# Performance work log

Hardware: AMD Instinct MI355X
Metric: run time of the kernel (lower is better)

The kernel has to match this reference:

```python
import jax, jax.numpy as jnp
import numpy as np

POOL = 7  # cfg.POOLING_SIZE


def roi_align_avg(feat, rois, scale):
    """Legacy RoIAlignAvg: bilinearly sample a (POOL+1)x(POOL+1) grid per RoI
    (crop_and_resize semantics: grid spans roi with divisor G-1), then 2x2
    average-pool with stride 1 -> POOL x POOL output. feat: [B,C,H,W]."""
    B, C, H, W = feat.shape
    G = POOL + 1
    b = rois[:, 0].astype(jnp.int32)                                  # [R]
    x1 = rois[:, 1] * scale
    y1 = rois[:, 2] * scale
    x2 = rois[:, 3] * scale
    y2 = rois[:, 4] * scale
    t = jnp.arange(G, dtype=feat.dtype) / (G - 1)                     # [G]
    ty = jnp.clip(y1[:, None] + (y2 - y1)[:, None] * t, 0.0, H - 1)   # [R,G] rows
    tx = jnp.clip(x1[:, None] + (x2 - x1)[:, None] * t, 0.0, W - 1)   # [R,G] cols
    y0f, x0f = jnp.floor(ty), jnp.floor(tx)
    wy = (ty - y0f)[:, :, None, None]                                 # row frac
    wx = (tx - x0f)[:, None, :, None]                                 # col frac
    y0 = y0f.astype(jnp.int32)
    x0 = x0f.astype(jnp.int32)
    y1i = jnp.minimum(y0 + 1, H - 1)
    x1i = jnp.minimum(x0 + 1, W - 1)

    def g(yi, xi):  # point gather -> [R,G,G,C]
        return feat[b[:, None, None], :, yi[:, :, None], xi[:, None, :]]

    v = ((1 - wy) * ((1 - wx) * g(y0, x0) + wx * g(y0, x1i))
         + wy * ((1 - wx) * g(y1i, x0) + wx * g(y1i, x1i)))           # [R,G,G,C]
    v = jnp.transpose(v, (0, 3, 1, 2))                                # [R,C,G,G]
    # 2x2 avg pool, stride 1 -> [R,C,POOL,POOL]
    return 0.25 * (v[:, :, :-1, :-1] + v[:, :, 1:, :-1]
                   + v[:, :, :-1, 1:] + v[:, :, 1:, 1:])


def reference(p2, p3, p4, p5, rois, im_info):
    """_PyramidRoI_Feat (POOLING_MODE='align'): data-dependent FPN level
    assignment per RoI, per-level RoIAlignAvg, reassembled in original RoI
    order (equivalent to the concat+sort in the torch code)."""
    h = rois[:, 4] - rois[:, 2] + 1.0
    w = rois[:, 3] - rois[:, 1] + 1.0
    lvl = jnp.floor(jnp.log(jnp.sqrt(h * w) / 224.0) / np.float32(np.log(2.0)) + 4.0)
    lvl = jnp.clip(lvl, 2.0, 5.0)                                     # [R]
    im_h = im_info[0, 0]
    out = 0.0
    for l, feat in zip((2, 3, 4, 5), (p2, p3, p4, p5)):
        scale = feat.shape[2] / im_h
        mask = (lvl == l).astype(feat.dtype)[:, None, None, None]
        out = out + mask * roi_align_avg(feat, rois, scale)
    return out  # [R, C, POOL, POOL]


def setup_inputs() -> dict:
    key = jax.random.key(0)
    ks = jax.random.split(key, 6)
    B, C = 1, 256
    IMH = IMW = 1024.0
    R = 2000
    p2 = jax.random.normal(ks[0], (B, C, 256, 256), jnp.float32)
    p3 = jax.random.normal(ks[1], (B, C, 128, 128), jnp.float32)
    p4 = jax.random.normal(ks[2], (B, C, 64, 64), jnp.float32)
    p5 = jax.random.normal(ks[3], (B, C, 32, 32), jnp.float32)
    # log-uniform box sizes so RoIs spread across all 4 pyramid levels
    wh = jnp.exp(jax.random.uniform(ks[4], (R, 2), jnp.float32,
                                    minval=np.log(16.0), maxval=np.log(600.0)))
    xy = jax.random.uniform(ks[5], (R, 2), jnp.float32) * (jnp.array([IMW, IMH]) - wh)
    rois = jnp.concatenate([
        jnp.zeros((R, 1), jnp.float32),            # batch index
        xy[:, 0:1], xy[:, 1:2],                    # x1, y1
        xy[:, 0:1] + wh[:, 0:1] - 1.0,             # x2
        xy[:, 1:2] + wh[:, 1:2] - 1.0,             # y2
    ], axis=1)
    im_info = jnp.array([[IMH, IMW, 1.0]], jnp.float32)
    return {"p2": p2, "p3": p3, "p4": p4, "p5": p5, "rois": rois, "im_info": im_info}
```

## Files before the change

kernel.cpp:

```cpp
#include <hip/hip_runtime.h>
#include <hip/hip_fp16.h>
#include <math.h>

#define POOLSZ 7
#define GRIDG 8
#define CCH  256
#define NBIN 256
#define OPP  (POOLSZ * POOLSZ)
#define MAXPER 8

typedef float fx4 __attribute__((ext_vector_type(4)));

__device__ __forceinline__ int roi_level(const float* __restrict__ rois, int r) {
    const float x1 = rois[r * 5 + 1];
    const float y1 = rois[r * 5 + 2];
    const float x2 = rois[r * 5 + 3];
    const float y2 = rois[r * 5 + 4];
    const float h = __fadd_rn(__fsub_rn(y2, y1), 1.0f);
    const float w = __fadd_rn(__fsub_rn(x2, x1), 1.0f);
    const float s = __fsqrt_rn(__fmul_rn(h, w));
    const float LOG2 = __uint_as_float(0x3F317218u);
    float lv = floorf(__fadd_rn(__fdiv_rn(logf(__fdiv_rn(s, 224.0f)), LOG2), 4.0f));
    lv = fminf(fmaxf(lv, 2.0f), 5.0f);
    return (int)lv;
}

__global__ __launch_bounds__(256) void prep_kernel(
    const float* __restrict__ p2, const float* __restrict__ p3,
    const float* __restrict__ p4, const float* __restrict__ p5,
    __half* __restrict__ t2, __half* __restrict__ t3,
    __half* __restrict__ t4, __half* __restrict__ t5,
    int HW2, int HW3, int HW4, int HW5,
    const float* __restrict__ rois, const float* __restrict__ im_info,
    int R, int* __restrict__ sorted, int nblkT)
{
    const int t = threadIdx.x;

    if ((int)blockIdx.x == nblkT) {
        __shared__ int cnt[NBIN];
        __shared__ int tmp[NBIN];
        cnt[t] = 0;
        __syncthreads();

        int myR[MAXPER], myBin[MAXPER], mySlot[MAXPER];
        int m = 0;
        const float ih = im_info[0], iw = im_info[1];
        for (int r = t; r < R && m < MAXPER; r += 256) {
            const int lvl = roi_level(rois, r);
            const float cx = 0.5f * (rois[r * 5 + 1] + rois[r * 5 + 3]);
            const float cy = 0.5f * (rois[r * 5 + 2] + rois[r * 5 + 4]);
            const int tx = min(7, max(0, (int)(cx * 8.0f / iw)));
            const int ty = min(7, max(0, (int)(cy * 8.0f / ih)));
            const int bin = (ty * 8 + tx) * 4 + (lvl - 2);
            myR[m] = r; myBin[m] = bin;
            mySlot[m] = atomicAdd(&cnt[bin], 1);
            ++m;
        }
        __syncthreads();

        const int v = cnt[t];
        tmp[t] = v;
        __syncthreads();
        for (int s = 1; s < NBIN; s <<= 1) {
            const int u = (t >= s) ? tmp[t - s] : 0;
            __syncthreads();
            tmp[t] += u;
            __syncthreads();
        }
        cnt[t] = tmp[t] - v;
        __syncthreads();

        for (int i = 0; i < m; ++i)
            sorted[cnt[myBin[i]] + mySlot[i]] = myR[i];
        return;
    }

    const int n2 = (HW2 / 64) * 4, n3 = (HW3 / 64) * 4, n4 = (HW4 / 64) * 4;
    int bid = blockIdx.x;
    const float* src; __half* dst; int HW;
    if (bid < n2)              { src = p2; dst = t2; HW = HW2; }
    else if ((bid -= n2) < n3) { src = p3; dst = t3; HW = HW3; }
    else if ((bid -= n3) < n4) { src = p4; dst = t4; HW = HW4; }
    else { bid -= n4;            src = p5; dst = t5; HW = HW5; }
    const int ptiles = HW / 64;
    const int pt = bid % ptiles, ct = bid / ptiles;
    const int pbase = pt * 64, cbase = ct * 64;

    __shared__ float tile[64][65];

    const int l = t & 15, cr = t >> 4;
#pragma unroll
    for (int p = 0; p < 4; ++p) {
        const int c = p * 16 + cr;
        const fx4* sp = (const fx4*)(src + (size_t)(cbase + c) * HW + pbase + l * 4);
        const fx4 v = __builtin_nontemporal_load(sp);
        tile[c][l * 4 + 0] = v.x;
        tile[c][l * 4 + 1] = v.y;
        tile[c][l * 4 + 2] = v.z;
        tile[c][l * 4 + 3] = v.w;
    }
    __syncthreads();

    const int ch2 = t & 31, pr = t >> 5;
#pragma unroll
    for (int p = 0; p < 8; ++p) {
        const int row = p * 8 + pr;
        const __half2 h = __floats2half2_rn(tile[ch2 * 2][row], tile[ch2 * 2 + 1][row]);
        *(__half2*)(dst + (size_t)(pbase + row) * CCH + cbase + ch2 * 2) = h;
    }
}

__global__ __launch_bounds__(256) void fpn_main_t(
    const __half* __restrict__ t2, const __half* __restrict__ t3,
    const __half* __restrict__ t4, const __half* __restrict__ t5,
    const float* __restrict__ rois, const float* __restrict__ im_info,
    float* __restrict__ out, const int* __restrict__ order,
    int H2, int H3, int H4, int H5, int R)
{
    const int n = blockIdx.x;
    const int q = R / 8, rem = R % 8;
    const int xcd = n % 8, idx = n / 8;
    const int nsw = (xcd < rem ? xcd * (q + 1) : rem * (q + 1) + (xcd - rem) * q) + idx;
    const int r = order ? order[nsw] : nsw;
    const int t = threadIdx.x;
    const int cpair = t & 127;
    const int grp   = t >> 7;
    const int c0    = cpair * 2;

    const float x1 = rois[r * 5 + 1];
    const float y1 = rois[r * 5 + 2];
    const float x2 = rois[r * 5 + 3];
    const float y2 = rois[r * 5 + 4];

    const int lvl = roi_level(rois, r);
    const __half* feat;
    int H;
    switch (lvl) {
        case 2:  feat = t2; H = H2; break;
        case 3:  feat = t3; H = H3; break;
        case 4:  feat = t4; H = H4; break;
        default: feat = t5; H = H5; break;
    }
    const int W = H;

    const float im_h  = im_info[0];
    const float scale = __fdiv_rn((float)H, im_h);
    const float ylo = __fmul_rn(y1, scale), yhi = __fmul_rn(y2, scale);
    const float xlo = __fmul_rn(x1, scale), xhi = __fmul_rn(x2, scale);

    float wx[GRIDG];
    int xoff[GRIDG], dxo[GRIDG];
#pragma unroll
    for (int i = 0; i < GRIDG; ++i) {
        const float tf = __fdiv_rn((float)i, (float)(GRIDG - 1));
        float tx = __fadd_rn(xlo, __fmul_rn(__fsub_rn(xhi, xlo), tf));
        tx = fminf(fmaxf(tx, 0.0f), (float)(W - 1));
        const float x0f = floorf(tx);
        const int   x0  = (int)x0f;
        xoff[i] = x0 * CCH;
        dxo[i]  = (min(x0 + 1, W - 1) - x0) * CCH;
        wx[i]   = __fsub_rn(tx, x0f);
    }

    float wyv[5];
    int yoff[5], dyo[5];
#pragma unroll
    for (int i = 0; i < 5; ++i) {
        const int gy = min(grp * 4 + i, GRIDG - 1);
        const float tf = __fdiv_rn((float)gy, (float)(GRIDG - 1));
        float ty = __fadd_rn(ylo, __fmul_rn(__fsub_rn(yhi, ylo), tf));
        ty = fminf(fmaxf(ty, 0.0f), (float)(H - 1));
        const float y0f = floorf(ty);
        const int   y0  = (int)y0f;
        yoff[i] = y0 * W * CCH;
        dyo[i]  = (min(y0 + 1, H - 1) - y0) * W * CCH;
        wyv[i]  = __fsub_rn(ty, y0f);
    }

    __shared__ float s_out[CCH * OPP];

    const __half* fb = feat + c0;
    float2 rowPrev[GRIDG], rowCur[GRIDG];
#pragma unroll
    for (int i = 0; i < 5; ++i) {
        if (grp == 1 && i == 4) break;
        const __half* base = fb + yoff[i];
        const int dyg = dyo[i];
        const float wyg = wyv[i];
        const float omy = 1.0f - wyg;
#pragma unroll
        for (int gx = 0; gx < GRIDG; ++gx) {
            const __half* qp = base + xoff[gx];
            const int dxg = dxo[gx];
            const float2 v00 = __half22float2(*(const __half2*)(qp));
            const float2 v01 = __half22float2(*(const __half2*)(qp + dxg));
            const float2 v10 = __half22float2(*(const __half2*)(qp + dyg));
            const float2 v11 = __half22float2(*(const __half2*)(qp + dyg + dxg));
            const float wxg = wx[gx];
            const float omx = 1.0f - wxg;
            rowCur[gx].x = omy * (omx * v00.x + wxg * v01.x)
                         + wyg * (omx * v10.x + wxg * v11.x);
            rowCur[gx].y = omy * (omx * v00.y + wxg * v01.y)
                         + wyg * (omx * v10.y + wxg * v11.y);
        }
        if (i > 0) {
            const int py = grp * 4 + i - 1;
#pragma unroll
            for (int px = 0; px < POOLSZ; ++px) {
                const float pvx = 0.25f * (rowPrev[px].x + rowPrev[px + 1].x
                                           + rowCur[px].x + rowCur[px + 1].x);
                const float pvy = 0.25f * (rowPrev[px].y + rowPrev[px + 1].y
                                           + rowCur[px].y + rowCur[px + 1].y);
                s_out[c0 * OPP + py * POOLSZ + px] = pvx;
                s_out[(c0 + 1) * OPP + py * POOLSZ + px] = pvy;
            }
        }
#pragma unroll
        for (int gx = 0; gx < GRIDG; ++gx) rowPrev[gx] = rowCur[gx];
    }

    __syncthreads();
    float* obase = out + (size_t)r * (CCH * OPP);
    const float* sp = s_out;
#pragma unroll
    for (int i = 0; i < 12; ++i) {
        const unsigned k4 = (unsigned)(i * 256 + t) * 4u;
        fx4 v;
        v.x = sp[k4 + 0]; v.y = sp[k4 + 1]; v.z = sp[k4 + 2]; v.w = sp[k4 + 3];
        __builtin_nontemporal_store(v, (fx4*)(obase + k4));
    }
    if (t < 64) {
        const unsigned k4 = (unsigned)(12 * 256 + t) * 4u;
        fx4 v;
        v.x = sp[k4 + 0]; v.y = sp[k4 + 1]; v.z = sp[k4 + 2]; v.w = sp[k4 + 3];
        __builtin_nontemporal_store(v, (fx4*)(obase + k4));
    }
}

__global__ __launch_bounds__(256) void fpn_roialign_kernel(
    const float* __restrict__ p2, const float* __restrict__ p3,
    const float* __restrict__ p4, const float* __restrict__ p5,
    const float* __restrict__ rois, const float* __restrict__ im_info,
    float* __restrict__ out,
    int H2, int H3, int H4, int H5, int R)
{
    const int r = blockIdx.x;

    const float bf = rois[r * 5 + 0];
    const float x1 = rois[r * 5 + 1];
    const float y1 = rois[r * 5 + 2];
    const float x2 = rois[r * 5 + 3];
    const float y2 = rois[r * 5 + 4];

    const int lvl = roi_level(rois, r);
    const float* feat;
    int H;
    switch (lvl) {
        case 2:  feat = p2; H = H2; break;
        case 3:  feat = p3; H = H3; break;
        case 4:  feat = p4; H = H4; break;
        default: feat = p5; H = H5; break;
    }
    const int W = H;
    const int wv  = threadIdx.x >> 6;
    const int lid = threadIdx.x & 63;
    const int gy  = lid >> 3;
    const int gx  = lid & 7;

    const float im_h  = im_info[0];
    const float scale = __fdiv_rn((float)H, im_h);
    const float ylo = __fmul_rn(y1, scale), yhi = __fmul_rn(y2, scale);
    const float xlo = __fmul_rn(x1, scale), xhi = __fmul_rn(x2, scale);
    float ty = __fadd_rn(ylo, __fmul_rn(__fsub_rn(yhi, ylo),
                                        __fdiv_rn((float)gy, (float)(GRIDG - 1))));
    ty = fminf(fmaxf(ty, 0.0f), (float)(H - 1));
    float tx = __fadd_rn(xlo, __fmul_rn(__fsub_rn(xhi, xlo),
                                        __fdiv_rn((float)gx, (float)(GRIDG - 1))));
    tx = fminf(fmaxf(tx, 0.0f), (float)(W - 1));
    const float y0f = floorf(ty), x0f = floorf(tx);
    const int   y0  = (int)y0f,   x0  = (int)x0f;
    const int   y1i = min(y0 + 1, H - 1);
    const int   x1i = min(x0 + 1, W - 1);
    const float wyv = __fsub_rn(ty, y0f);
    const float wxv = __fsub_rn(tx, x0f);
    const float omy = 1.0f - wyv;
    const float omx = 1.0f - wxv;

    const int b = (int)bf;
    const size_t plane = (size_t)H * W;
    const float* fbase = feat + (size_t)(b * CCH + wv * 64) * plane;
    const int o00 = y0  * W + x0;
    const int o01 = y0  * W + x1i;
    const int o10 = y1i * W + x0;
    const int o11 = y1i * W + x1i;

    float* obase = out + (size_t)r * (CCH * OPP) + (size_t)(wv * 64) * OPP;
    const bool wr  = (gy < POOLSZ) && (gx < POOLSZ);
    const int oidx = gy * POOLSZ + gx;

#pragma unroll 4
    for (int k = 0; k < 64; ++k) {
        const float* f = fbase + (size_t)k * plane;
        const float v00 = f[o00];
        const float v01 = f[o01];
        const float v10 = f[o10];
        const float v11 = f[o11];
        const float v = omy * (omx * v00 + wxv * v01) + wyv * (omx * v10 + wxv * v11);
        const float vb  = __shfl_down(v, 8);
        const float vr  = __shfl_down(v, 1);
        const float vbr = __shfl_down(v, 9);
        if (wr) obase[k * OPP + oidx] = 0.25f * (((v + vb) + vr) + vbr);
    }
}

extern "C" void kernel_launch(void* const* d_in, const int* in_sizes, int n_in,
                              void* d_out, int out_size, void* d_ws, size_t ws_size,
                              hipStream_t stream) {
    const float* p2      = (const float*)d_in[0];
    const float* p3      = (const float*)d_in[1];
    const float* p4      = (const float*)d_in[2];
    const float* p5      = (const float*)d_in[3];
    const float* rois    = (const float*)d_in[4];
    const float* im_info = (const float*)d_in[5];
    float* out = (float*)d_out;

    const int R = in_sizes[4] / 5;
    auto dimOf = [](int sz) {
        int hw = sz / CCH;
        return (int)(sqrtf((float)hw) + 0.5f);
    };
    const int H2 = dimOf(in_sizes[0]);
    const int H3 = dimOf(in_sizes[1]);
    const int H4 = dimOf(in_sizes[2]);
    const int H5 = dimOf(in_sizes[3]);
    const size_t HW2 = (size_t)H2 * H2, HW3 = (size_t)H3 * H3;
    const size_t HW4 = (size_t)H4 * H4, HW5 = (size_t)H5 * H5;

    const size_t sortBytes = (size_t)R * sizeof(int);
    const size_t sortPad   = (sortBytes + 255) & ~(size_t)255;
    const size_t transBytes = (HW2 + HW3 + HW4 + HW5) * CCH * sizeof(__half);
    const bool canSort  = (ws_size >= sortBytes) && (R <= 256 * MAXPER);
    const bool canTrans = ws_size >= sortPad + transBytes;

    if (canTrans) {
        int* sorted = canSort ? (int*)d_ws : nullptr;
        __half* t2 = (__half*)((char*)d_ws + sortPad);
        __half* t3 = t2 + HW2 * CCH;
        __half* t4 = t3 + HW3 * CCH;
        __half* t5 = t4 + HW4 * CCH;
        const int nblkT = (int)((HW2 + HW3 + HW4 + HW5) / 64 * 4);
        const int nblk  = nblkT + (canSort ? 1 : 0);
        prep_kernel<<<nblk, 256, 0, stream>>>(
            p2, p3, p4, p5, t2, t3, t4, t5,
            (int)HW2, (int)HW3, (int)HW4, (int)HW5,
            rois, im_info, R, sorted, nblkT);
        fpn_main_t<<<R, 256, 0, stream>>>(
            t2, t3, t4, t5, rois, im_info, out, sorted, H2, H3, H4, H5, R);
    } else {
        fpn_roialign_kernel<<<R, 256, 0, stream>>>(
            p2, p3, p4, p5, rois, im_info, out, H2, H3, H4, H5, R);
    }
}
```

Before: 62.07 us.

## Split prep into three kernels to overlap p2 transpose with coarse-level RoI work

The single prep kernel plus main kernel becomes three launches. The first sorts RoIs level-major and transposes p3-p5 to fp16 NHWC. The second interleaves p2 tile transposes with RoIAlign blocks for level 3-5 RoIs, and the third handles level-2 RoIs once p2 is ready. The aim is to hide the large p2 conversion behind useful RoI work rather than serializing all conversion before any sampling. The cost is an extra launch, idle early-exit blocks in k2 and k3, and a changed sort key that groups RoIs by level first.

```diff
diff --git a/kernel.cpp b/kernel.cpp
--- a/kernel.cpp
+++ b/kernel.cpp
@@ -25,104 +25,82 @@
     return (int)lv;
 }
 
-__global__ __launch_bounds__(256) void prep_kernel(
-    const float* __restrict__ p2, const float* __restrict__ p3,
-    const float* __restrict__ p4, const float* __restrict__ p5,
-    __half* __restrict__ t2, __half* __restrict__ t3,
-    __half* __restrict__ t4, __half* __restrict__ t5,
-    int HW2, int HW3, int HW4, int HW5,
-    const float* __restrict__ rois, const float* __restrict__ im_info,
-    int R, int* __restrict__ sorted, int nblkT)
-{
-    const int t = threadIdx.x;
-
-    if ((int)blockIdx.x == nblkT) {
-        __shared__ int cnt[NBIN];
-        __shared__ int tmp[NBIN];
-        cnt[t] = 0;
+__device__ __forceinline__ void do_sort(const float* __restrict__ rois,
+                                        const float* __restrict__ im_info,
+                                        int R, int* __restrict__ sorted,
+                                        int* __restrict__ meta, char* lds, int t)
+{
+    int* cnt = (int*)lds;
+    int* tmp = cnt + NBIN;
+    cnt[t] = 0;
+    __syncthreads();
+    int myR[MAXPER], myBin[MAXPER], mySlot[MAXPER];
+    int m = 0;
+    const float ih = im_info[0], iw = im_info[1];
+    for (int r = t; r < R && m < MAXPER; r += 256) {
+        const int lvl = roi_level(rois, r);
+        const float cx = 0.5f * (rois[r * 5 + 1] + rois[r * 5 + 3]);
+        const float cy = 0.5f * (rois[r * 5 + 2] + rois[r * 5 + 4]);
+        const int tx = min(7, max(0, (int)(cx * 8.0f / iw)));
+        const int ty = min(7, max(0, (int)(cy * 8.0f / ih)));
+        const int bin = (lvl - 2) * 64 + ty * 8 + tx;
+        myR[m] = r; myBin[m] = bin;
+        mySlot[m] = atomicAdd(&cnt[bin], 1);
+        ++m;
+    }
+    __syncthreads();
+    const int v = cnt[t];
+    tmp[t] = v;
+    __syncthreads();
+    for (int s = 1; s < NBIN; s <<= 1) {
+        const int u = (t >= s) ? tmp[t - s] : 0;
         __syncthreads();
-
-        int myR[MAXPER], myBin[MAXPER], mySlot[MAXPER];
-        int m = 0;
-        const float ih = im_info[0], iw = im_info[1];
-        for (int r = t; r < R && m < MAXPER; r += 256) {
-            const int lvl = roi_level(rois, r);
-            const float cx = 0.5f * (rois[r * 5 + 1] + rois[r * 5 + 3]);
-            const float cy = 0.5f * (rois[r * 5 + 2] + rois[r * 5 + 4]);
-            const int tx = min(7, max(0, (int)(cx * 8.0f / iw)));
-            const int ty = min(7, max(0, (int)(cy * 8.0f / ih)));
-            const int bin = (ty * 8 + tx) * 4 + (lvl - 2);
-            myR[m] = r; myBin[m] = bin;
-            mySlot[m] = atomicAdd(&cnt[bin], 1);
-            ++m;
-        }
+        tmp[t] += u;
         __syncthreads();
-
-        const int v = cnt[t];
-        tmp[t] = v;
-        __syncthreads();
-        for (int s = 1; s < NBIN; s <<= 1) {
-            const int u = (t >= s) ? tmp[t - s] : 0;
-            __syncthreads();
-            tmp[t] += u;
-            __syncthreads();
-        }
-        cnt[t] = tmp[t] - v;
-        __syncthreads();
-
-        for (int i = 0; i < m; ++i)
-            sorted[cnt[myBin[i]] + mySlot[i]] = myR[i];
-        return;
-    }
-
-    const int n2 = (HW2 / 64) * 4, n3 = (HW3 / 64) * 4, n4 = (HW4 / 64) * 4;
-    int bid = blockIdx.x;
-    const float* src; __half* dst; int HW;
-    if (bid < n2)              { src = p2; dst = t2; HW = HW2; }
-    else if ((bid -= n2) < n3) { src = p3; dst = t3; HW = HW3; }
-    else if ((bid -= n3) < n4) { src = p4; dst = t4; HW = HW4; }
-    else { bid -= n4;            src = p5; dst = t5; HW = HW5; }
+    }
+    cnt[t] = tmp[t] - v;
+    if (t == 64) meta[0] = cnt[64];
+    __syncthreads();
+    for (int i = 0; i < m; ++i)
+        sorted[cnt[myBin[i]] + mySlot[i]] = myR[i];
+}
+
+__device__ __forceinline__ void do_tile(const float* __restrict__ src,
+                                        __half* __restrict__ dst,
+                                        int HW, int jj, int t, char* lds)
+{
+    float* tile = (float*)lds;
     const int ptiles = HW / 64;
-    const int pt = bid % ptiles, ct = bid / ptiles;
+    const int pt = jj % ptiles, ct = jj / ptiles;
     const int pbase = pt * 64, cbase = ct * 64;
-
-    __shared__ float tile[64][65];
-
     const int l = t & 15, cr = t >> 4;
 #pragma unroll
     for (int p = 0; p < 4; ++p) {
         const int c = p * 16 + cr;
         const fx4* sp = (const fx4*)(src + (size_t)(cbase + c) * HW + pbase + l * 4);
         const fx4 v = __builtin_nontemporal_load(sp);
-        tile[c][l * 4 + 0] = v.x;
-        tile[c][l * 4 + 1] = v.y;
-        tile[c][l * 4 + 2] = v.z;
-        tile[c][l * 4 + 3] = v.w;
-    }
-    __syncthreads();
-
+        tile[c * 65 + l * 4 + 0] = v.x;
+        tile[c * 65 + l * 4 + 1] = v.y;
+        tile[c * 65 + l * 4 + 2] = v.z;
+        tile[c * 65 + l * 4 + 3] = v.w;
+    }
+    __syncthreads();
     const int ch2 = t & 31, pr = t >> 5;
 #pragma unroll
     for (int p = 0; p < 8; ++p) {
         const int row = p * 8 + pr;
-        const __half2 h = __floats2half2_rn(tile[ch2 * 2][row], tile[ch2 * 2 + 1][row]);
+        const __half2 h = __floats2half2_rn(tile[(ch2 * 2) * 65 + row],
+                                            tile[(ch2 * 2 + 1) * 65 + row]);
         *(__half2*)(dst + (size_t)(pbase + row) * CCH + cbase + ch2 * 2) = h;
     }
 }
 
-__global__ __launch_bounds__(256) void fpn_main_t(
-    const __half* __restrict__ t2, const __half* __restrict__ t3,
-    const __half* __restrict__ t4, const __half* __restrict__ t5,
+__device__ __forceinline__ void process_roi(
+    int r, const __half* __restrict__ feat, int H,
     const float* __restrict__ rois, const float* __restrict__ im_info,
-    float* __restrict__ out, const int* __restrict__ order,
-    int H2, int H3, int H4, int H5, int R)
-{
-    const int n = blockIdx.x;
-    const int q = R / 8, rem = R % 8;
-    const int xcd = n % 8, idx = n / 8;
-    const int nsw = (xcd < rem ? xcd * (q + 1) : rem * (q + 1) + (xcd - rem) * q) + idx;
-    const int r = order ? order[nsw] : nsw;
-    const int t = threadIdx.x;
+    float* __restrict__ out, char* lds, int t)
+{
+    const int W = H;
     const int cpair = t & 127;
     const int grp   = t >> 7;
     const int c0    = cpair * 2;
@@ -131,18 +109,6 @@
     const float y1 = rois[r * 5 + 2];
     const float x2 = rois[r * 5 + 3];
     const float y2 = rois[r * 5 + 4];
-
-    const int lvl = roi_level(rois, r);
-    const __half* feat;
-    int H;
-    switch (lvl) {
-        case 2:  feat = t2; H = H2; break;
-        case 3:  feat = t3; H = H3; break;
-        case 4:  feat = t4; H = H4; break;
-        default: feat = t5; H = H5; break;
-    }
-    const int W = H;
-
     const float im_h  = im_info[0];
     const float scale = __fdiv_rn((float)H, im_h);
     const float ylo = __fmul_rn(y1, scale), yhi = __fmul_rn(y2, scale);
@@ -177,7 +143,7 @@
         wyv[i]  = __fsub_rn(ty, y0f);
     }
 
-    __shared__ float s_out[CCH * OPP];
+    float* s_out = (float*)lds;
 
     const __half* fb = feat + c0;
     float2 rowPrev[GRIDG], rowCur[GRIDG];
@@ -237,6 +203,80 @@
     }
 }
 
+__global__ __launch_bounds__(256) void k1_kernel(
+    const float* __restrict__ p3, const float* __restrict__ p4,
+    const float* __restrict__ p5,
+    __half* __restrict__ t3, __half* __restrict__ t4, __half* __restrict__ t5,
+    int HW3, int HW4, int HW5,
+    const float* __restrict__ rois, const float* __restrict__ im_info,
+    int R, int* __restrict__ sorted, int* __restrict__ meta)
+{
+    __shared__ __align__(16) char lds[64 * 65 * 4];
+    const int t = threadIdx.x;
+    if (blockIdx.x == 0) {
+        do_sort(rois, im_info, R, sorted, meta, lds, t);
+        return;
+    }
+    int j = blockIdx.x - 1;
+    const int n5t = (HW5 / 64) * 4, n4t = (HW4 / 64) * 4;
+    if (j < n5t)                { do_tile(p5, t5, HW5, j, t, lds); return; }
+    if ((j -= n5t) < n4t)       { do_tile(p4, t4, HW4, j, t, lds); return; }
+    do_tile(p3, t3, HW3, j - n4t, t, lds);
+}
+
+__global__ __launch_bounds__(256) void k2_kernel(
+    const float* __restrict__ p2, __half* __restrict__ t2, int HW2,
+    const __half* __restrict__ t3, const __half* __restrict__ t4,
+    const __half* __restrict__ t5,
+    const float* __restrict__ rois, const float* __restrict__ im_info,
+    float* __restrict__ out, const int* __restrict__ sorted,
+    const int* __restrict__ meta,
+    int R, int H2, int H3, int H4, int H5)
+{
+    __shared__ __align__(16) char lds[CCH * OPP * 4];
+    const int t = threadIdx.x;
+    const long long NA = (HW2 / 64) * 4;
+    const long long N  = NA + R;
+    const long long i  = blockIdx.x;
+    const long long a0 = (i * NA) / N;
+    const long long a1 = ((i + 1) * NA) / N;
+    if (a1 > a0) {
+        do_tile(p2, t2, HW2, (int)a0, t, lds);
+        return;
+    }
+    const int k = (int)(i - a0);
+    const int n2 = meta[0];
+    const int n345 = R - n2;
+    if (k >= n345) return;
+    const int r = sorted[n2 + k];
+    const int lvl = roi_level(rois, r);
+    const __half* feat; int H;
+    switch (lvl) {
+        case 2:  feat = t2; H = H2; break;
+        case 3:  feat = t3; H = H3; break;
+        case 4:  feat = t4; H = H4; break;
+        default: feat = t5; H = H5; break;
+    }
+    process_roi(r, feat, H, rois, im_info, out, lds, t);
+}
+
+__global__ __launch_bounds__(256) void k3_kernel(
+    const __half* __restrict__ t2, int H2,
+    const float* __restrict__ rois, const float* __restrict__ im_info,
+    float* __restrict__ out, const int* __restrict__ sorted,
+    const int* __restrict__ meta, int R)
+{
+    __shared__ __align__(16) char lds[CCH * OPP * 4];
+    const int n2 = meta[0];
+    const int k = blockIdx.x;
+    if (k >= n2) return;
+    const int q = n2 / 8, rem = n2 % 8;
+    const int xcd = k % 8, idx = k / 8;
+    const int swz = (xcd < rem ? xcd * (q + 1) : rem * (q + 1) + (xcd - rem) * q) + idx;
+    const int r = sorted[swz];
+    process_roi(r, t2, H2, rois, im_info, out, lds, (int)threadIdx.x);
+}
+
 __global__ __launch_bounds__(256) void fpn_roialign_kernel(
     const float* __restrict__ p2, const float* __restrict__ p3,
     const float* __restrict__ p4, const float* __restrict__ p5,
@@ -245,7 +285,6 @@
     int H2, int H3, int H4, int H5, int R)
 {
     const int r = blockIdx.x;
-
     const float bf = rois[r * 5 + 0];
     const float x1 = rois[r * 5 + 1];
     const float y1 = rois[r * 5 + 2];
@@ -336,26 +375,31 @@
     const size_t HW2 = (size_t)H2 * H2, HW3 = (size_t)H3 * H3;
     const size_t HW4 = (size_t)H4 * H4, HW5 = (size_t)H5 * H5;
 
-    const size_t sortBytes = (size_t)R * sizeof(int);
-    const size_t sortPad   = (sortBytes + 255) & ~(size_t)255;
+    const size_t metaPad   = 256;
+    const size_t sortPad   = ((size_t)R * sizeof(int) + 255) & ~(size_t)255;
     const size_t transBytes = (HW2 + HW3 + HW4 + HW5) * CCH * sizeof(__half);
-    const bool canSort  = (ws_size >= sortBytes) && (R <= 256 * MAXPER);
-    const bool canTrans = ws_size >= sortPad + transBytes;
-
-    if (canTrans) {
-        int* sorted = canSort ? (int*)d_ws : nullptr;
-        __half* t2 = (__half*)((char*)d_ws + sortPad);
+    const bool canRun = (ws_size >= metaPad + sortPad + transBytes) && (R <= 256 * MAXPER);
+
+    if (canRun) {
+        int* meta   = (int*)d_ws;
+        int* sorted = (int*)((char*)d_ws + metaPad);
+        __half* t2 = (__half*)((char*)d_ws + metaPad + sortPad);
         __half* t3 = t2 + HW2 * CCH;
         __half* t4 = t3 + HW3 * CCH;
         __half* t5 = t4 + HW4 * CCH;
-        const int nblkT = (int)((HW2 + HW3 + HW4 + HW5) / 64 * 4);
-        const int nblk  = nblkT + (canSort ? 1 : 0);
-        prep_kernel<<<nblk, 256, 0, stream>>>(
-            p2, p3, p4, p5, t2, t3, t4, t5,
-            (int)HW2, (int)HW3, (int)HW4, (int)HW5,
-            rois, im_info, R, sorted, nblkT);
-        fpn_main_t<<<R, 256, 0, stream>>>(
-            t2, t3, t4, t5, rois, im_info, out, sorted, H2, H3, H4, H5, R);
+        const int n5t = (int)(HW5 / 64) * 4;
+        const int n4t = (int)(HW4 / 64) * 4;
+        const int n3t = (int)(HW3 / 64) * 4;
+        const int n2t = (int)(HW2 / 64) * 4;
+
+        k1_kernel<<<1 + n5t + n4t + n3t, 256, 0, stream>>>(
+            p3, p4, p5, t3, t4, t5, (int)HW3, (int)HW4, (int)HW5,
+            rois, im_info, R, sorted, meta);
+        k2_kernel<<<n2t + R, 256, 0, stream>>>(
+            p2, t2, (int)HW2, t3, t4, t5, rois, im_info, out, sorted, meta,
+            R, H2, H3, H4, H5);
+        k3_kernel<<<R, 256, 0, stream>>>(
+            t2, H2, rois, im_info, out, sorted, meta, R);
     } else {
         fpn_roialign_kernel<<<R, 256, 0, stream>>>(
             p2, p3, p4, p5, rois, im_info, out, H2, H3, H4, H5, R);
```

Result: slower. 77.65 us (+25.1%).

## Convert RoI main kernel to persistent blocks with atomic work queue

Applied to the files above, without the earlier changes.

Replaces the one-block-per-RoI launch with a persistent kernel of 768 blocks that pull sorted RoI indices from a global atomic counter, which is reset by a memset before the prep kernel. The goal is to balance the uneven per-level work dynamically and cut block launch overhead. It drops the XCD-aware swizzle of block indices, so locality across chiplets now depends on the dynamic order in which blocks claim work. It also adds an atomic plus two barriers per RoI and an extra memset call.

```diff
diff --git a/kernel.cpp b/kernel.cpp
--- a/kernel.cpp
+++ b/kernel.cpp
@@ -25,104 +25,81 @@
     return (int)lv;
 }
 
-__global__ __launch_bounds__(256) void prep_kernel(
-    const float* __restrict__ p2, const float* __restrict__ p3,
-    const float* __restrict__ p4, const float* __restrict__ p5,
-    __half* __restrict__ t2, __half* __restrict__ t3,
-    __half* __restrict__ t4, __half* __restrict__ t5,
-    int HW2, int HW3, int HW4, int HW5,
-    const float* __restrict__ rois, const float* __restrict__ im_info,
-    int R, int* __restrict__ sorted, int nblkT)
-{
-    const int t = threadIdx.x;
-
-    if ((int)blockIdx.x == nblkT) {
-        __shared__ int cnt[NBIN];
-        __shared__ int tmp[NBIN];
-        cnt[t] = 0;
+__device__ __forceinline__ void do_sort(const float* __restrict__ rois,
+                                        const float* __restrict__ im_info,
+                                        int R, int* __restrict__ sorted,
+                                        char* lds, int t)
+{
+    int* cnt = (int*)lds;
+    int* tmp = cnt + NBIN;
+    cnt[t] = 0;
+    __syncthreads();
+    int myR[MAXPER], myBin[MAXPER], mySlot[MAXPER];
+    int m = 0;
+    const float ih = im_info[0], iw = im_info[1];
+    for (int r = t; r < R && m < MAXPER; r += 256) {
+        const int lvl = roi_level(rois, r);
+        const float cx = 0.5f * (rois[r * 5 + 1] + rois[r * 5 + 3]);
+        const float cy = 0.5f * (rois[r * 5 + 2] + rois[r * 5 + 4]);
+        const int tx = min(7, max(0, (int)(cx * 8.0f / iw)));
+        const int ty = min(7, max(0, (int)(cy * 8.0f / ih)));
+        const int bin = (ty * 8 + tx) * 4 + (lvl - 2);
+        myR[m] = r; myBin[m] = bin;
+        mySlot[m] = atomicAdd(&cnt[bin], 1);
+        ++m;
+    }
+    __syncthreads();
+    const int v = cnt[t];
+    tmp[t] = v;
+    __syncthreads();
+    for (int s = 1; s < NBIN; s <<= 1) {
+        const int u = (t >= s) ? tmp[t - s] : 0;
         __syncthreads();
-
-        int myR[MAXPER], myBin[MAXPER], mySlot[MAXPER];
-        int m = 0;
-        const float ih = im_info[0], iw = im_info[1];
-        for (int r = t; r < R && m < MAXPER; r += 256) {
-            const int lvl = roi_level(rois, r);
-            const float cx = 0.5f * (rois[r * 5 + 1] + rois[r * 5 + 3]);
-            const float cy = 0.5f * (rois[r * 5 + 2] + rois[r * 5 + 4]);
-            const int tx = min(7, max(0, (int)(cx * 8.0f / iw)));
-            const int ty = min(7, max(0, (int)(cy * 8.0f / ih)));
-            const int bin = (ty * 8 + tx) * 4 + (lvl - 2);
-            myR[m] = r; myBin[m] = bin;
-            mySlot[m] = atomicAdd(&cnt[bin], 1);
-            ++m;
-        }
+        tmp[t] += u;
         __syncthreads();
-
-        const int v = cnt[t];
-        tmp[t] = v;
-        __syncthreads();
-        for (int s = 1; s < NBIN; s <<= 1) {
-            const int u = (t >= s) ? tmp[t - s] : 0;
-            __syncthreads();
-            tmp[t] += u;
-            __syncthreads();
-        }
-        cnt[t] = tmp[t] - v;
-        __syncthreads();
-
-        for (int i = 0; i < m; ++i)
-            sorted[cnt[myBin[i]] + mySlot[i]] = myR[i];
-        return;
-    }
-
-    const int n2 = (HW2 / 64) * 4, n3 = (HW3 / 64) * 4, n4 = (HW4 / 64) * 4;
-    int bid = blockIdx.x;
-    const float* src; __half* dst; int HW;
-    if (bid < n2)              { src = p2; dst = t2; HW = HW2; }
-    else if ((bid -= n2) < n3) { src = p3; dst = t3; HW = HW3; }
-    else if ((bid -= n3) < n4) { src = p4; dst = t4; HW = HW4; }
-    else { bid -= n4;            src = p5; dst = t5; HW = HW5; }
+    }
+    cnt[t] = tmp[t] - v;
+    __syncthreads();
+    for (int i = 0; i < m; ++i)
+        sorted[cnt[myBin[i]] + mySlot[i]] = myR[i];
+}
+
+__device__ __forceinline__ void do_tile(const float* __restrict__ src,
+                                        __half* __restrict__ dst,
+                                        int HW, int jj, int t, char* lds)
+{
+    float* tile = (float*)lds;
     const int ptiles = HW / 64;
-    const int pt = bid % ptiles, ct = bid / ptiles;
+    const int pt = jj % ptiles, ct = jj / ptiles;
     const int pbase = pt * 64, cbase = ct * 64;
-
-    __shared__ float tile[64][65];
-
     const int l = t & 15, cr = t >> 4;
 #pragma unroll
     for (int p = 0; p < 4; ++p) {
         const int c = p * 16 + cr;
         const fx4* sp = (const fx4*)(src + (size_t)(cbase + c) * HW + pbase + l * 4);
         const fx4 v = __builtin_nontemporal_load(sp);
-        tile[c][l * 4 + 0] = v.x;
-        tile[c][l * 4 + 1] = v.y;
-        tile[c][l * 4 + 2] = v.z;
-        tile[c][l * 4 + 3] = v.w;
-    }
-    __syncthreads();
-
+        tile[c * 65 + l * 4 + 0] = v.x;
+        tile[c * 65 + l * 4 + 1] = v.y;
+        tile[c * 65 + l * 4 + 2] = v.z;
+        tile[c * 65 + l * 4 + 3] = v.w;
+    }
+    __syncthreads();
     const int ch2 = t & 31, pr = t >> 5;
 #pragma unroll
     for (int p = 0; p < 8; ++p) {
         const int row = p * 8 + pr;
-        const __half2 h = __floats2half2_rn(tile[ch2 * 2][row], tile[ch2 * 2 + 1][row]);
+        const __half2 h = __floats2half2_rn(tile[(ch2 * 2) * 65 + row],
+                                            tile[(ch2 * 2 + 1) * 65 + row]);
         *(__half2*)(dst + (size_t)(pbase + row) * CCH + cbase + ch2 * 2) = h;
     }
 }
 
-__global__ __launch_bounds__(256) void fpn_main_t(
-    const __half* __restrict__ t2, const __half* __restrict__ t3,
-    const __half* __restrict__ t4, const __half* __restrict__ t5,
+__device__ __forceinline__ void process_roi(
+    int r, const __half* __restrict__ feat, int H,
     const float* __restrict__ rois, const float* __restrict__ im_info,
-    float* __restrict__ out, const int* __restrict__ order,
-    int H2, int H3, int H4, int H5, int R)
-{
-    const int n = blockIdx.x;
-    const int q = R / 8, rem = R % 8;
-    const int xcd = n % 8, idx = n / 8;
-    const int nsw = (xcd < rem ? xcd * (q + 1) : rem * (q + 1) + (xcd - rem) * q) + idx;
-    const int r = order ? order[nsw] : nsw;
-    const int t = threadIdx.x;
+    float* __restrict__ out, char* lds, int t)
+{
+    const int W = H;
     const int cpair = t & 127;
     const int grp   = t >> 7;
     const int c0    = cpair * 2;
@@ -131,18 +108,6 @@
     const float y1 = rois[r * 5 + 2];
     const float x2 = rois[r * 5 + 3];
     const float y2 = rois[r * 5 + 4];
-
-    const int lvl = roi_level(rois, r);
-    const __half* feat;
-    int H;
-    switch (lvl) {
-        case 2:  feat = t2; H = H2; break;
-        case 3:  feat = t3; H = H3; break;
-        case 4:  feat = t4; H = H4; break;
-        default: feat = t5; H = H5; break;
-    }
-    const int W = H;
-
     const float im_h  = im_info[0];
     const float scale = __fdiv_rn((float)H, im_h);
     const float ylo = __fmul_rn(y1, scale), yhi = __fmul_rn(y2, scale);
@@ -177,7 +142,7 @@
         wyv[i]  = __fsub_rn(ty, y0f);
     }
 
-    __shared__ float s_out[CCH * OPP];
+    float* s_out = (float*)lds;
 
     const __half* fb = feat + c0;
     float2 rowPrev[GRIDG], rowCur[GRIDG];
@@ -237,6 +202,61 @@
     }
 }
 
+__global__ __launch_bounds__(256) void prep_kernel(
+    const float* __restrict__ p2, const float* __restrict__ p3,
+    const float* __restrict__ p4, const float* __restrict__ p5,
+    __half* __restrict__ t2, __half* __restrict__ t3,
+    __half* __restrict__ t4, __half* __restrict__ t5,
+    int HW2, int HW3, int HW4, int HW5,
+    const float* __restrict__ rois, const float* __restrict__ im_info,
+    int R, int* __restrict__ sorted, int nblkT)
+{
+    __shared__ __align__(16) char lds[64 * 65 * 4];
+    const int t = threadIdx.x;
+    if ((int)blockIdx.x == nblkT) {
+        do_sort(rois, im_info, R, sorted, lds, t);
+        return;
+    }
+    const int n2 = (HW2 / 64) * 4, n3 = (HW3 / 64) * 4, n4 = (HW4 / 64) * 4;
+    int bid = blockIdx.x;
+    const float* src; __half* dst; int HW;
+    if (bid < n2)              { src = p2; dst = t2; HW = HW2; }
+    else if ((bid -= n2) < n3) { src = p3; dst = t3; HW = HW3; }
+    else if ((bid -= n3) < n4) { src = p4; dst = t4; HW = HW4; }
+    else { bid -= n4;            src = p5; dst = t5; HW = HW5; }
+    do_tile(src, dst, HW, bid, t, lds);
+}
+
+__global__ __launch_bounds__(256) void fpn_main_persist(
+    const __half* __restrict__ t2, const __half* __restrict__ t3,
+    const __half* __restrict__ t4, const __half* __restrict__ t5,
+    const float* __restrict__ rois, const float* __restrict__ im_info,
+    float* __restrict__ out, const int* __restrict__ sorted,
+    int* __restrict__ ctr,
+    int H2, int H3, int H4, int H5, int R)
+{
+    __shared__ __align__(16) char lds[CCH * OPP * 4];
+    __shared__ int sh;
+    const int t = threadIdx.x;
+    for (;;) {
+        if (t == 0) sh = atomicAdd(ctr, 1);
+        __syncthreads();
+        const int n = sh;
+        if (n >= R) return;
+        const int r = sorted ? sorted[n] : n;
+        const int lvl = roi_level(rois, r);
+        const __half* feat; int H;
+        switch (lvl) {
+            case 2:  feat = t2; H = H2; break;
+            case 3:  feat = t3; H = H3; break;
+            case 4:  feat = t4; H = H4; break;
+            default: feat = t5; H = H5; break;
+        }
+        process_roi(r, feat, H, rois, im_info, out, lds, t);
+        __syncthreads();
+    }
+}
+
 __global__ __launch_bounds__(256) void fpn_roialign_kernel(
     const float* __restrict__ p2, const float* __restrict__ p3,
     const float* __restrict__ p4, const float* __restrict__ p5,
@@ -245,16 +265,13 @@
     int H2, int H3, int H4, int H5, int R)
 {
     const int r = blockIdx.x;
-
     const float bf = rois[r * 5 + 0];
     const float x1 = rois[r * 5 + 1];
     const float y1 = rois[r * 5 + 2];
     const float x2 = rois[r * 5 + 3];
     const float y2 = rois[r * 5 + 4];
-
     const int lvl = roi_level(rois, r);
-    const float* feat;
-    int H;
+    const float* feat; int H;
     switch (lvl) {
         case 2:  feat = p2; H = H2; break;
         case 3:  feat = p3; H = H3; break;
@@ -266,7 +283,6 @@
     const int lid = threadIdx.x & 63;
     const int gy  = lid >> 3;
     const int gx  = lid & 7;
-
     const float im_h  = im_info[0];
     const float scale = __fdiv_rn((float)H, im_h);
     const float ylo = __fmul_rn(y1, scale), yhi = __fmul_rn(y2, scale);
@@ -285,7 +301,6 @@
     const float wxv = __fsub_rn(tx, x0f);
     const float omy = 1.0f - wyv;
     const float omx = 1.0f - wxv;
-
     const int b = (int)bf;
     const size_t plane = (size_t)H * W;
     const float* fbase = feat + (size_t)(b * CCH + wv * 64) * plane;
@@ -293,11 +308,9 @@
     const int o01 = y0  * W + x1i;
     const int o10 = y1i * W + x0;
     const int o11 = y1i * W + x1i;
-
     float* obase = out + (size_t)r * (CCH * OPP) + (size_t)(wv * 64) * OPP;
     const bool wr  = (gy < POOLSZ) && (gx < POOLSZ);
     const int oidx = gy * POOLSZ + gx;
-
 #pragma unroll 4
     for (int k = 0; k < 64; ++k) {
         const float* f = fbase + (size_t)k * plane;
@@ -336,28 +349,33 @@
     const size_t HW2 = (size_t)H2 * H2, HW3 = (size_t)H3 * H3;
     const size_t HW4 = (size_t)H4 * H4, HW5 = (size_t)H5 * H5;
 
-    const size_t sortBytes = (size_t)R * sizeof(int);
-    const size_t sortPad   = (sortBytes + 255) & ~(size_t)255;
+    const size_t ctrPad    = 256;
+    const size_t sortPad   = ((size_t)R * sizeof(int) + 255) & ~(size_t)255;
     const size_t transBytes = (HW2 + HW3 + HW4 + HW5) * CCH * sizeof(__half);
-    const bool canSort  = (ws_size >= sortBytes) && (R <= 256 * MAXPER);
-    const bool canTrans = ws_size >= sortPad + transBytes;
-
-    if (canTrans) {
-        int* sorted = canSort ? (int*)d_ws : nullptr;
-        __half* t2 = (__half*)((char*)d_ws + sortPad);
-        __half* t3 = t2 + HW2 * CCH;
-        __half* t4 = t3 + HW3 * CCH;
-        __half* t5 = t4 + HW4 * CCH;
-        const int nblkT = (int)((HW2 + HW3 + HW4 + HW5) / 64 * 4);
-        const int nblk  = nblkT + (canSort ? 1 : 0);
-        prep_kernel<<<nblk, 256, 0, stream>>>(
-            p2, p3, p4, p5, t2, t3, t4, t5,
-            (int)HW2, (int)HW3, (int)HW4, (int)HW5,
-            rois, im_info, R, sorted, nblkT);
-        fpn_main_t<<<R, 256, 0, stream>>>(
-            t2, t3, t4, t5, rois, im_info, out, sorted, H2, H3, H4, H5, R);
-    } else {
+    const bool canSort = (R <= 256 * MAXPER);
+    const bool canRun  = ws_size >= ctrPad + sortPad + transBytes;
+
+    if (!canRun) {
         fpn_roialign_kernel<<<R, 256, 0, stream>>>(
             p2, p3, p4, p5, rois, im_info, out, H2, H3, H4, H5, R);
-    }
-}
+        return;
+    }
+
+    int* ctr    = (int*)d_ws;
+    int* sorted = canSort ? (int*)((char*)d_ws + ctrPad) : nullptr;
+    __half* t2 = (__half*)((char*)d_ws + ctrPad + sortPad);
+    __half* t3 = t2 + HW2 * CCH;
+    __half* t4 = t3 + HW3 * CCH;
+    __half* t5 = t4 + HW4 * CCH;
+
+    hipMemsetAsync(ctr, 0, sizeof(int), stream);
+    const int nblkT = (int)((HW2 + HW3 + HW4 + HW5) / 64 * 4);
+    prep_kernel<<<nblkT + (canSort ? 1 : 0), 256, 0, stream>>>(
+        p2, p3, p4, p5, t2, t3, t4, t5,
+        (int)HW2, (int)HW3, (int)HW4, (int)HW5,
+        rois, im_info, R, sorted, nblkT);
+
+    const int NPERSIST = 768;
+    fpn_main_persist<<<NPERSIST, 256, 0, stream>>>(
+        t2, t3, t4, t5, rois, im_info, out, sorted, ctr, H2, H3, H4, H5, R);
+}
```

Result: slower. 79.19 us (+27.6%).
